# Optimization experiments

Hardware: AMD Instinct MI355X
Metric: run time of the kernel (lower is better)

The kernel has to match this reference:

```python
import jax, jax.numpy as jnp
import numpy as np

DIM = 256
HEADS = 4
HEAD_DIM = DIM // HEADS
MLP_HIDDEN = DIM * 3
B, N = 8, 4096
EPS = 1e-5


def setup_inputs() -> dict:
    key = jax.random.key(0)
    ks = jax.random.split(key, 8)
    s = 0.02
    return {
        "x": jax.random.normal(ks[0], (B, N, DIM), dtype=jnp.float32),
        "w_qkv": jax.random.normal(ks[1], (DIM, 3 * DIM), dtype=jnp.float32) * s,
        "b_qkv": jnp.zeros((3 * DIM,), dtype=jnp.float32),
        "norm_g": jnp.ones((DIM,), dtype=jnp.float32),
        "norm_b": jnp.zeros((DIM,), dtype=jnp.float32),
        "w_fc1": jax.random.normal(ks[2], (DIM, MLP_HIDDEN), dtype=jnp.float32) * s,
        "b_fc1": jnp.zeros((MLP_HIDDEN,), dtype=jnp.float32),
        "w_fc2": jax.random.normal(ks[3], (MLP_HIDDEN, DIM), dtype=jnp.float32) * s,
        "b_fc2": jnp.zeros((DIM,), dtype=jnp.float32),
    }


def _layernorm(x, g, b):
    mu = jnp.mean(x, axis=-1, keepdims=True)
    var = jnp.mean(jnp.square(x - mu), axis=-1, keepdims=True)
    return (x - mu) * jax.lax.rsqrt(var + EPS) * g + b


def reference(x, w_qkv, b_qkv, norm_g, norm_b, w_fc1, b_fc1, w_fc2, b_fc2):
    Bx, Nx, C = x.shape
    scale = HEAD_DIM ** -0.5
    qkv = (x @ w_qkv + b_qkv).reshape(Bx, Nx, 3, HEADS, HEAD_DIM)
    qkv = jnp.transpose(qkv, (2, 0, 3, 1, 4))  # [3, B, H, N, hd]
    q, k, v = qkv[0], qkv[1], qkv[2]
    k = k * scale
    # channel attention: [B,H,hd,hd]
    attn = jnp.einsum('bhnd,bhne->bhde', k, v)
    attn = jax.nn.softmax(attn, axis=-1)
    # x_feature[b,h,n,d] = sum_e attn[b,h,d,e] * q[b,h,n,e]
    xf = jnp.einsum('bhde,bhne->bhnd', attn, q)
    xf = jnp.transpose(xf, (0, 2, 1, 3)).reshape(Bx, Nx, C)
    x = x + xf
    # FFN with residual (exact GELU as torch nn.GELU default)
    h = _layernorm(x, norm_g, norm_b)
    h = jax.nn.gelu(h @ w_fc1 + b_fc1, approximate=False) @ w_fc2 + b_fc2
    return x + h
```

## Files before the change

kernel.cpp:

```cpp
#include <hip/hip_runtime.h>
#include <math.h>

typedef __bf16 bf16_t;
typedef __bf16 bf16x4 __attribute__((ext_vector_type(4)));
typedef __bf16 bf16x8 __attribute__((ext_vector_type(8)));
typedef float f32x4 __attribute__((ext_vector_type(4)));

#define DIMC 256
#define HID 768
#define NB 8
#define NN 4096
#define ROWS (NB*NN)
#define NCHUNK 16

#define AS1 __attribute__((address_space(1)))
#define AS3 __attribute__((address_space(3)))

__device__ __forceinline__ void gll16(const bf16_t* src, void* lds) {
  __builtin_amdgcn_global_load_lds((const AS1 void*)src, (AS3 void*)lds, 16, 0, 0);
}

__global__ __launch_bounds__(256) void prep_x_kernel(const float* __restrict__ x,
                                                     bf16_t* __restrict__ xb) {
  int i = (blockIdx.x * 256 + threadIdx.x) * 8;
  f32x4 a = *(const f32x4*)(x + i);
  f32x4 b = *(const f32x4*)(x + i + 4);
  bf16x8 o;
  o[0] = (bf16_t)a[0]; o[1] = (bf16_t)a[1]; o[2] = (bf16_t)a[2]; o[3] = (bf16_t)a[3];
  o[4] = (bf16_t)b[0]; o[5] = (bf16_t)b[1]; o[6] = (bf16_t)b[2]; o[7] = (bf16_t)b[3];
  *(bf16x8*)(xb + i) = o;
}

__global__ __launch_bounds__(256)
void pack_w_kernel(const float* __restrict__ w, bf16_t* __restrict__ out,
                   int K, int Nw) {
  int idx = blockIdx.x * 256 + threadIdx.x;
  int lane = idx & 63;
  int kq = (idx >> 6) % (K >> 5);
  int nt = idx / ((K >> 5) << 6);
  int n = nt * 16 + (lane & 15);
  int k0 = kq * 32 + (lane >> 4) * 8;
  bf16x8 o;
#pragma unroll
  for (int j = 0; j < 8; ++j) o[j] = (bf16_t)w[(size_t)(k0 + j) * Nw + n];
  *(bf16x8*)(out + (size_t)idx * 8) = o;
}

__device__ __forceinline__ float gelu_exact(float v) {
  return 0.5f * v * (1.0f + erff(v * 0.70710678118654752f));
}

template <int EPI>
__global__ __launch_bounds__(256, 2)
void gemm_packed_kernel(const bf16_t* __restrict__ A, const bf16_t* __restrict__ Bp,
                        const float* __restrict__ bias, bf16_t* __restrict__ outp) {
  __shared__ __align__(16) unsigned char smem[32768];
  const int tid = threadIdx.x;
  const int d = blockIdx.x + blockIdx.y * 4;
  const int w_ = (d & 7) * 256 + (d >> 3);
  const int panel = w_ & 3, rowb = w_ >> 2;
  const int m0 = rowb * 64;
  const int n0 = panel * 192;
  const int lane = tid & 63, w = tid >> 6;
  const int lr = lane & 15, lk = lane >> 4;

#pragma unroll
  for (int i = 0; i < 8; ++i) {
    int idx = i * 256 + tid;
    int row = idx >> 5, pk = idx & 31;
    gll16(A + (size_t)(m0 + row) * 256 + ((pk ^ (row & 7)) * 8), smem + idx * 16);
  }
  asm volatile("s_waitcnt vmcnt(0)" ::: "memory");
  __builtin_amdgcn_s_barrier();

  f32x4 acc[4][3] = {};
  const bf16_t* bb = Bp + (size_t)((panel * 12 + w * 3) * 8) * 512 + lane * 8;

  bf16x8 bf_c[3], af_c[4], bf_n[3], af_n[4];
#pragma unroll
  for (int nf = 0; nf < 3; ++nf) bf_c[nf] = *(const bf16x8*)(bb + (nf * 8) * 512);
#pragma unroll
  for (int mi = 0; mi < 4; ++mi) {
    int row = mi * 16 + lr;
    af_c[mi] = *(const bf16x8*)(smem + row * 512 + ((lk ^ (row & 7)) * 16));
  }

#pragma unroll
  for (int kq = 0; kq < 8; ++kq) {
    if (kq < 7) {
#pragma unroll
      for (int nf = 0; nf < 3; ++nf)
        bf_n[nf] = *(const bf16x8*)(bb + (nf * 8 + kq + 1) * 512);
#pragma unroll
      for (int mi = 0; mi < 4; ++mi) {
        int row = mi * 16 + lr;
        af_n[mi] = *(const bf16x8*)(smem + row * 512 + ((((kq + 1) * 4 + lk) ^ (row & 7)) * 16));
      }
    }
    __builtin_amdgcn_s_setprio(1);
#pragma unroll
    for (int nf = 0; nf < 3; ++nf)
#pragma unroll
      for (int mi = 0; mi < 4; ++mi)
        acc[mi][nf] = __builtin_amdgcn_mfma_f32_16x16x32_bf16(bf_c[nf], af_c[mi],
                                                              acc[mi][nf], 0, 0, 0);
    __builtin_amdgcn_s_setprio(0);
#pragma unroll
    for (int nf = 0; nf < 3; ++nf) bf_c[nf] = bf_n[nf];
#pragma unroll
    for (int mi = 0; mi < 4; ++mi) af_c[mi] = af_n[mi];
  }

  f32x4 bs[3];
#pragma unroll
  for (int nf = 0; nf < 3; ++nf)
    bs[nf] = *(const f32x4*)(bias + n0 + w * 48 + nf * 16 + lk * 4);

  __syncthreads();
#pragma unroll
  for (int mi = 0; mi < 4; ++mi) {
    int row_l = mi * 16 + lr;
#pragma unroll
    for (int nf = 0; nf < 3; ++nf) {
      int col = w * 48 + nf * 16 + lk * 4;
      f32x4 v = acc[mi][nf] + bs[nf];
      bf16x4 o;
#pragma unroll
      for (int r = 0; r < 4; ++r) {
        float val = v[r];
        if (EPI == 1) val = gelu_exact(val);
        o[r] = (bf16_t)val;
      }
      int chunk = col >> 3;
      int half = (col >> 2) & 1;
      *(bf16x4*)(smem + row_l * 384 + ((chunk ^ (row_l & 7)) << 4) + (half << 3)) = o;
    }
  }
  __syncthreads();
#pragma unroll
  for (int i = 0; i < 6; ++i) {
    int id = i * 256 + tid;
    int row_l = id / 24, c = id % 24;
    bf16x8 v = *(const bf16x8*)(smem + row_l * 384 + ((c ^ (row_l & 7)) << 4));
    *(bf16x8*)(outp + (size_t)(m0 + row_l) * 768 + n0 + c * 8) = v;
  }
}

__global__ __launch_bounds__(256, 2)
void fc2_packed_kernel(const bf16_t* __restrict__ mid, const bf16_t* __restrict__ Bp,
                       const float* __restrict__ bias, const bf16_t* __restrict__ resid,
                       float* __restrict__ outp) {
  __shared__ __align__(16) unsigned char smem[2 * 16384 + 32768];
  unsigned char* epi = smem + 32768;
  const int tid = threadIdx.x;
  const int m0 = blockIdx.x * 64;
  const int lane = tid & 63, w = tid >> 6;
  const int lr = lane & 15, lk = lane >> 4;

  auto stageA = [&](int c, int buf) {
#pragma unroll
    for (int i = 0; i < 4; ++i) {
      int idx = i * 256 + tid;
      int row = idx >> 4, pk = idx & 15;
      gll16(mid + (size_t)(m0 + row) * 768 + c * 128 + ((pk ^ (row & 7)) * 8),
            smem + buf * 16384 + idx * 16);
    }
  };

  stageA(0, 0);
  stageA(1, 1);
  asm volatile("s_waitcnt vmcnt(4)" ::: "memory");
  __builtin_amdgcn_s_barrier();

  f32x4 acc[4][4] = {};
#pragma unroll
  for (int c = 0; c < 6; ++c) {
    bf16x8 bf[4][4];
#pragma unroll
    for (int nf = 0; nf < 4; ++nf)
#pragma unroll
      for (int kql = 0; kql < 4; ++kql)
        bf[nf][kql] = *(const bf16x8*)(Bp + (size_t)((w * 4 + nf) * 24 + c * 4 + kql) * 512 + lane * 8);
    asm volatile("s_waitcnt vmcnt(0)" ::: "memory");
    __builtin_amdgcn_s_barrier();
#pragma unroll
    for (int kql = 0; kql < 4; ++kql) {
#pragma unroll
      for (int mi = 0; mi < 4; ++mi) {
        int row = mi * 16 + lr;
        bf16x8 a8 = *(const bf16x8*)(smem + (c & 1) * 16384 + row * 256 +
                                     (((kql * 4 + lk) ^ (row & 7)) * 16));
#pragma unroll
        for (int nf = 0; nf < 4; ++nf)
          acc[mi][nf] = __builtin_amdgcn_mfma_f32_16x16x32_bf16(bf[nf][kql], a8, acc[mi][nf], 0, 0, 0);
      }
    }
    __builtin_amdgcn_s_barrier();
    if (c + 2 < 6) stageA(c + 2, c & 1);
  }

  f32x4 bs[4];
#pragma unroll
  for (int nf = 0; nf < 4; ++nf)
    bs[nf] = *(const f32x4*)(bias + w * 64 + nf * 16 + lk * 4);

#pragma unroll
  for (int ph = 0; ph < 2; ++ph) {
    if (ph == 1) __syncthreads();
#pragma unroll
    for (int mj = 0; mj < 2; ++mj) {
      int mi = ph * 2 + mj;
      int row_l = mj * 16 + lr;
#pragma unroll
      for (int nf = 0; nf < 4; ++nf) {
        int cc = w * 64 + nf * 16 + lk * 4;
        f32x4 v = acc[mi][nf] + bs[nf];
        int chunk = cc >> 2;
        *(f32x4*)(epi + row_l * 1024 + ((chunk ^ (row_l & 7)) << 4)) = v;
      }
    }
    __syncthreads();
#pragma unroll
    for (int i = 0; i < 8; ++i) {
      int id = i * 256 + tid;
      int rl = id >> 6, c = id & 63;
      f32x4 v = *(const f32x4*)(epi + rl * 1024 + ((c ^ (rl & 7)) << 4));
      int grow = m0 + ph * 32 + rl;
      bf16x4 rz = *(const bf16x4*)(resid + (size_t)grow * 256 + c * 4);
#pragma unroll
      for (int r = 0; r < 4; ++r) v[r] += (float)rz[r];
      *(f32x4*)(outp + (size_t)grow * 256 + c * 4) = v;
    }
  }
}

__global__ __launch_bounds__(256)
void attn_kv_kernel(const bf16_t* __restrict__ qkv, float* __restrict__ part) {
  const int bh = blockIdx.x, chunk = blockIdx.y;
  const int b = bh >> 2, h = bh & 3;
  __shared__ __align__(16) float kl[32][68];
  __shared__ __align__(16) float vl[32][68];
  const int tid = threadIdx.x;
  const int dg = tid >> 4, eg = tid & 15;
  f32x4 acc[4] = {};
  const int n00 = chunk * (NN / NCHUNK);
  const int srow = tid >> 3, spk = tid & 7;
  for (int t = 0; t < (NN / NCHUNK) / 32; ++t) {
    int n0 = n00 + t * 32;
    {
      const bf16x8 k8 = *(const bf16x8*)(qkv + (size_t)(b * NN + n0 + srow) * HID + 256 + h * 64 + spk * 8);
      const bf16x8 v8 = *(const bf16x8*)(qkv + (size_t)(b * NN + n0 + srow) * HID + 512 + h * 64 + spk * 8);
#pragma unroll
      for (int j = 0; j < 8; ++j) kl[srow][spk * 8 + j] = (float)k8[j];
#pragma unroll
      for (int j = 0; j < 8; ++j) vl[srow][spk * 8 + j] = (float)v8[j];
    }
    __syncthreads();
#pragma unroll 8
    for (int n = 0; n < 32; ++n) {
      f32x4 k4 = *(const f32x4*)&kl[n][dg * 4];
      f32x4 v4 = *(const f32x4*)&vl[n][eg * 4];
#pragma unroll
      for (int i = 0; i < 4; ++i) acc[i] += k4[i] * v4;
    }
    __syncthreads();
  }
  float* dst = part + (size_t)(chunk * 32 + bh) * 4096;
#pragma unroll
  for (int i = 0; i < 4; ++i)
    *(f32x4*)&dst[(dg * 4 + i) * 64 + eg * 4] = acc[i];
}

__global__ __launch_bounds__(256)
void attn_softmax_kernel(const float* __restrict__ part, bf16_t* __restrict__ attnb) {
  const int bh = blockIdx.x;
  const int tid = threadIdx.x;
  const int dg = tid >> 4, eg = tid & 15;
  f32x4 s[4] = {};
  for (int c = 0; c < NCHUNK; ++c) {
    const float* src = part + (size_t)(c * 32 + bh) * 4096;
#pragma unroll
    for (int i = 0; i < 4; ++i) s[i] += *(const f32x4*)&src[(dg * 4 + i) * 64 + eg * 4];
  }
  bf16_t* dst = attnb + (size_t)bh * 4096;
#pragma unroll
  for (int i = 0; i < 4; ++i) {
    f32x4 l = s[i] * 0.125f;
    float m = fmaxf(fmaxf(l[0], l[1]), fmaxf(l[2], l[3]));
#pragma unroll
    for (int msk = 1; msk < 16; msk <<= 1) m = fmaxf(m, __shfl_xor(m, msk));
    f32x4 p;
    float sum = 0.f;
#pragma unroll
    for (int j = 0; j < 4; ++j) { p[j] = expf(l[j] - m); sum += p[j]; }
#pragma unroll
    for (int msk = 1; msk < 16; msk <<= 1) sum += __shfl_xor(sum, msk);
    float inv = 1.0f / sum;
    bf16x4 o;
#pragma unroll
    for (int j = 0; j < 4; ++j) o[j] = (bf16_t)(p[j] * inv);
    *(bf16x4*)&dst[(dg * 4 + i) * 64 + eg * 4] = o;
  }
}

__global__ __launch_bounds__(256, 2)
void xf_ln_mfma_kernel(const bf16_t* __restrict__ qkv, const bf16_t* __restrict__ attnb,
                       const bf16_t* __restrict__ xb, bf16_t* __restrict__ x2b,
                       bf16_t* __restrict__ hln, const float* __restrict__ gamma,
                       const float* __restrict__ beta) {
  __shared__ __align__(16) unsigned char qs[32768];
  __shared__ float red[4][4][16][2];
  const int tid = threadIdx.x;
  const int row0 = blockIdx.x * 64;
  const int b = row0 >> 12;
  const int lane = tid & 63, h = tid >> 6;
  const int lr = lane & 15, lk = lane >> 4;

#pragma unroll
  for (int i = 0; i < 8; ++i) {
    int idx = i * 256 + tid;
    int row = idx >> 5, pk = idx & 31;
    gll16(qkv + (size_t)(row0 + row) * HID + ((pk ^ (row & 7)) * 8), qs + idx * 16);
  }
  asm volatile("s_waitcnt vmcnt(0)" ::: "memory");
  __builtin_amdgcn_s_barrier();

  bf16x8 af[4][2];
#pragma unroll
  for (int mi = 0; mi < 4; ++mi)
#pragma unroll
    for (int kk = 0; kk < 2; ++kk) {
      int row = mi * 16 + lr;
      int pk = h * 8 + kk * 4 + lk;
      af[mi][kk] = *(const bf16x8*)(qs + row * 512 + ((pk ^ (row & 7)) * 16));
    }
  bf16x8 bfr[4][2];
#pragma unroll
  for (int nf = 0; nf < 4; ++nf)
#pragma unroll
    for (int kk = 0; kk < 2; ++kk)
      bfr[nf][kk] = *(const bf16x8*)(attnb + (size_t)(b * 4 + h) * 4096 +
                                     (nf * 16 + lr) * 64 + kk * 32 + lk * 8);
  f32x4 acc[4][4] = {};
#pragma unroll
  for (int kk = 0; kk < 2; ++kk)
#pragma unroll
    for (int mi = 0; mi < 4; ++mi)
#pragma unroll
      for (int nf = 0; nf < 4; ++nf)
        acc[mi][nf] = __builtin_amdgcn_mfma_f32_16x16x32_bf16(bfr[nf][kk], af[mi][kk], acc[mi][nf], 0, 0, 0);

  float ps[4], pq[4];
#pragma unroll
  for (int mi = 0; mi < 4; ++mi) {
    ps[mi] = 0.f; pq[mi] = 0.f;
    int row = row0 + mi * 16 + lr;
#pragma unroll
    for (int nf = 0; nf < 4; ++nf) {
      int col = h * 64 + nf * 16 + lk * 4;
      size_t off = (size_t)row * DIMC + col;
      bf16x4 xv = *(const bf16x4*)(xb + off);
      f32x4 x2;
#pragma unroll
      for (int r = 0; r < 4; ++r) {
        x2[r] = acc[mi][nf][r] + (float)xv[r];
        ps[mi] += x2[r]; pq[mi] += x2[r] * x2[r];
      }
      acc[mi][nf] = x2;
      bf16x4 o;
#pragma unroll
      for (int r = 0; r < 4; ++r) o[r] = (bf16_t)x2[r];
      *(bf16x4*)(x2b + off) = o;
    }
#pragma unroll
    for (int m = 16; m < 64; m <<= 1) {
      ps[mi] += __shfl_xor(ps[mi], m);
      pq[mi] += __shfl_xor(pq[mi], m);
    }
  }
  if (lk == 0) {
#pragma unroll
    for (int mi = 0; mi < 4; ++mi) { red[h][mi][lr][0] = ps[mi]; red[h][mi][lr][1] = pq[mi]; }
  }
  __builtin_amdgcn_s_barrier();
#pragma unroll
  for (int mi = 0; mi < 4; ++mi) {
    float t1 = red[0][mi][lr][0] + red[1][mi][lr][0] + red[2][mi][lr][0] + red[3][mi][lr][0];
    float t2 = red[0][mi][lr][1] + red[1][mi][lr][1] + red[2][mi][lr][1] + red[3][mi][lr][1];
    float mu = t1 * (1.0f / 256.0f);
    float var = t2 * (1.0f / 256.0f) - mu * mu;
    float rs = rsqrtf(var + 1e-5f);
    int row = row0 + mi * 16 + lr;
#pragma unroll
    for (int nf = 0; nf < 4; ++nf) {
      int col = h * 64 + nf * 16 + lk * 4;
      f32x4 g4 = *(const f32x4*)(gamma + col);
      f32x4 b4 = *(const f32x4*)(beta + col);
      bf16x4 o;
#pragma unroll
      for (int r = 0; r < 4; ++r)
        o[r] = (bf16_t)((acc[mi][nf][r] - mu) * rs * g4[r] + b4[r]);
      *(bf16x4*)(hln + (size_t)row * DIMC + col) = o;
    }
  }
}

extern "C" void kernel_launch(void* const* d_in, const int* in_sizes, int n_in,
                              void* d_out, int out_size, void* d_ws, size_t ws_size,
                              hipStream_t stream) {
  const float* x      = (const float*)d_in[0];
  const float* w_qkv  = (const float*)d_in[1];
  const float* b_qkv  = (const float*)d_in[2];
  const float* norm_g = (const float*)d_in[3];
  const float* norm_b = (const float*)d_in[4];
  const float* w_fc1  = (const float*)d_in[5];
  const float* b_fc1  = (const float*)d_in[6];
  const float* w_fc2  = (const float*)d_in[7];
  const float* b_fc2  = (const float*)d_in[8];

  char* ws = (char*)d_ws;
  size_t off = 0;
  bf16_t* qkv   = (bf16_t*)(ws + off); off += (size_t)ROWS * HID * 2;
  bf16_t* mid   = qkv;
  bf16_t* xb    = (bf16_t*)(ws + off); off += (size_t)ROWS * DIMC * 2;
  bf16_t* hln   = (bf16_t*)(ws + off); off += (size_t)ROWS * DIMC * 2;
  bf16_t* x2b   = (bf16_t*)(ws + off); off += (size_t)ROWS * DIMC * 2;
  float*  part  = (float*)(ws + off);  off += (size_t)NCHUNK * 32 * 4096 * 4;
  bf16_t* attnb = (bf16_t*)(ws + off); off += (size_t)32 * 4096 * 2;
  bf16_t* Bq    = (bf16_t*)(ws + off); off += (size_t)768 * 256 * 2;
  bf16_t* B1    = (bf16_t*)(ws + off); off += (size_t)768 * 256 * 2;
  bf16_t* B2    = (bf16_t*)(ws + off); off += (size_t)256 * 768 * 2;

  prep_x_kernel<<<(ROWS * DIMC) / (256 * 8), 256, 0, stream>>>(x, xb);
  pack_w_kernel<<<96, 256, 0, stream>>>(w_qkv, Bq, 256, 768);
  pack_w_kernel<<<96, 256, 0, stream>>>(w_fc1, B1, 256, 768);
  pack_w_kernel<<<96, 256, 0, stream>>>(w_fc2, B2, 768, 256);

  gemm_packed_kernel<0><<<dim3(4, ROWS / 64), 256, 0, stream>>>(xb, Bq, b_qkv, qkv);
  attn_kv_kernel<<<dim3(32, NCHUNK), 256, 0, stream>>>(qkv, part);
  attn_softmax_kernel<<<32, 256, 0, stream>>>(part, attnb);
  xf_ln_mfma_kernel<<<ROWS / 64, 256, 0, stream>>>(qkv, attnb, xb, x2b, hln, norm_g, norm_b);
  gemm_packed_kernel<1><<<dim3(4, ROWS / 64), 256, 0, stream>>>(hln, B1, b_fc1, mid);
  fc2_packed_kernel<<<ROWS / 64, 256, 0, stream>>>(mid, B2, b_fc2, x2b, (float*)d_out);
}
```

Measured before the change: 130.4 us.

## Fuse prep kernels, deepen B-fragment prefetch in GEMM, double attention chunks

Merges the x-to-bf16 conversion and the three weight-packing kernels into a single launch, removing three kernel launches and their gaps. The packed GEMM now prefetches B fragments two k-steps ahead using a triple-buffered register array instead of copying next-to-current each step, which is meant to hide global-load latency. NCHUNK is raised from 16 to 32, doubling the parallelism of the KV-reduction kernel but also the size of the partial buffer the softmax kernel has to reduce. Register pressure in the GEMM rises, which could hurt occupancy at the two-blocks-per-SIMD launch bound.

```diff
diff --git a/kernel.cpp b/kernel.cpp
--- a/kernel.cpp
+++ b/kernel.cpp
@@ -11,7 +11,7 @@
 #define NB 8
 #define NN 4096
 #define ROWS (NB*NN)
-#define NCHUNK 16
+#define NCHUNK 32
 
 #define AS1 __attribute__((address_space(1)))
 #define AS3 __attribute__((address_space(3)))
@@ -20,21 +20,12 @@
   __builtin_amdgcn_global_load_lds((const AS1 void*)src, (AS3 void*)lds, 16, 0, 0);
 }
 
-__global__ __launch_bounds__(256) void prep_x_kernel(const float* __restrict__ x,
-                                                     bf16_t* __restrict__ xb) {
-  int i = (blockIdx.x * 256 + threadIdx.x) * 8;
-  f32x4 a = *(const f32x4*)(x + i);
-  f32x4 b = *(const f32x4*)(x + i + 4);
-  bf16x8 o;
-  o[0] = (bf16_t)a[0]; o[1] = (bf16_t)a[1]; o[2] = (bf16_t)a[2]; o[3] = (bf16_t)a[3];
-  o[4] = (bf16_t)b[0]; o[5] = (bf16_t)b[1]; o[6] = (bf16_t)b[2]; o[7] = (bf16_t)b[3];
-  *(bf16x8*)(xb + i) = o;
-}
-
-__global__ __launch_bounds__(256)
-void pack_w_kernel(const float* __restrict__ w, bf16_t* __restrict__ out,
-                   int K, int Nw) {
-  int idx = blockIdx.x * 256 + threadIdx.x;
+__device__ __forceinline__ float gelu_exact(float v) {
+  return 0.5f * v * (1.0f + erff(v * 0.70710678118654752f));
+}
+
+__device__ __forceinline__ void pack_w_body(int idx, const float* __restrict__ w,
+                                            bf16_t* __restrict__ out, int K, int Nw) {
   int lane = idx & 63;
   int kq = (idx >> 6) % (K >> 5);
   int nt = idx / ((K >> 5) << 6);
@@ -46,8 +37,27 @@
   *(bf16x8*)(out + (size_t)idx * 8) = o;
 }
 
-__device__ __forceinline__ float gelu_exact(float v) {
-  return 0.5f * v * (1.0f + erff(v * 0.70710678118654752f));
+__global__ __launch_bounds__(256)
+void prep_all_kernel(const float* __restrict__ x, bf16_t* __restrict__ xb,
+                     const float* __restrict__ w_qkv, bf16_t* __restrict__ Bq,
+                     const float* __restrict__ w_fc1, bf16_t* __restrict__ B1,
+                     const float* __restrict__ w_fc2, bf16_t* __restrict__ B2) {
+  const int bid = blockIdx.x, tid = threadIdx.x;
+  if (bid < 4096) {
+    int i = (bid * 256 + tid) * 8;
+    f32x4 a = *(const f32x4*)(x + i);
+    f32x4 b = *(const f32x4*)(x + i + 4);
+    bf16x8 o;
+    o[0] = (bf16_t)a[0]; o[1] = (bf16_t)a[1]; o[2] = (bf16_t)a[2]; o[3] = (bf16_t)a[3];
+    o[4] = (bf16_t)b[0]; o[5] = (bf16_t)b[1]; o[6] = (bf16_t)b[2]; o[7] = (bf16_t)b[3];
+    *(bf16x8*)(xb + i) = o;
+  } else if (bid < 4192) {
+    pack_w_body((bid - 4096) * 256 + tid, w_qkv, Bq, 256, 768);
+  } else if (bid < 4288) {
+    pack_w_body((bid - 4192) * 256 + tid, w_fc1, B1, 256, 768);
+  } else {
+    pack_w_body((bid - 4288) * 256 + tid, w_fc2, B2, 768, 256);
+  }
 }
 
 template <int EPI>
@@ -76,25 +86,32 @@
   f32x4 acc[4][3] = {};
   const bf16_t* bb = Bp + (size_t)((panel * 12 + w * 3) * 8) * 512 + lane * 8;
 
-  bf16x8 bf_c[3], af_c[4], bf_n[3], af_n[4];
-#pragma unroll
-  for (int nf = 0; nf < 3; ++nf) bf_c[nf] = *(const bf16x8*)(bb + (nf * 8) * 512);
+  bf16x8 bf[3][3];
+  bf16x8 af[2][4];
+#pragma unroll
+  for (int nf = 0; nf < 3; ++nf) {
+    bf[0][nf] = *(const bf16x8*)(bb + (nf * 8 + 0) * 512);
+    bf[1][nf] = *(const bf16x8*)(bb + (nf * 8 + 1) * 512);
+  }
 #pragma unroll
   for (int mi = 0; mi < 4; ++mi) {
     int row = mi * 16 + lr;
-    af_c[mi] = *(const bf16x8*)(smem + row * 512 + ((lk ^ (row & 7)) * 16));
+    af[0][mi] = *(const bf16x8*)(smem + row * 512 + ((lk ^ (row & 7)) * 16));
   }
 
 #pragma unroll
   for (int kq = 0; kq < 8; ++kq) {
+    if (kq < 6) {
+#pragma unroll
+      for (int nf = 0; nf < 3; ++nf)
+        bf[(kq + 2) % 3][nf] = *(const bf16x8*)(bb + (nf * 8 + kq + 2) * 512);
+    }
     if (kq < 7) {
-#pragma unroll
-      for (int nf = 0; nf < 3; ++nf)
-        bf_n[nf] = *(const bf16x8*)(bb + (nf * 8 + kq + 1) * 512);
 #pragma unroll
       for (int mi = 0; mi < 4; ++mi) {
         int row = mi * 16 + lr;
-        af_n[mi] = *(const bf16x8*)(smem + row * 512 + ((((kq + 1) * 4 + lk) ^ (row & 7)) * 16));
+        af[(kq + 1) & 1][mi] =
+            *(const bf16x8*)(smem + row * 512 + ((((kq + 1) * 4 + lk) ^ (row & 7)) * 16));
       }
     }
     __builtin_amdgcn_s_setprio(1);
@@ -102,13 +119,9 @@
     for (int nf = 0; nf < 3; ++nf)
 #pragma unroll
       for (int mi = 0; mi < 4; ++mi)
-        acc[mi][nf] = __builtin_amdgcn_mfma_f32_16x16x32_bf16(bf_c[nf], af_c[mi],
+        acc[mi][nf] = __builtin_amdgcn_mfma_f32_16x16x32_bf16(bf[kq % 3][nf], af[kq & 1][mi],
                                                               acc[mi][nf], 0, 0, 0);
     __builtin_amdgcn_s_setprio(0);
-#pragma unroll
-    for (int nf = 0; nf < 3; ++nf) bf_c[nf] = bf_n[nf];
-#pragma unroll
-    for (int mi = 0; mi < 4; ++mi) af_c[mi] = af_n[mi];
   }
 
   f32x4 bs[3];
@@ -431,10 +444,7 @@
   bf16_t* B1    = (bf16_t*)(ws + off); off += (size_t)768 * 256 * 2;
   bf16_t* B2    = (bf16_t*)(ws + off); off += (size_t)256 * 768 * 2;
 
-  prep_x_kernel<<<(ROWS * DIMC) / (256 * 8), 256, 0, stream>>>(x, xb);
-  pack_w_kernel<<<96, 256, 0, stream>>>(w_qkv, Bq, 256, 768);
-  pack_w_kernel<<<96, 256, 0, stream>>>(w_fc1, B1, 256, 768);
-  pack_w_kernel<<<96, 256, 0, stream>>>(w_fc2, B2, 768, 256);
+  prep_all_kernel<<<4384, 256, 0, stream>>>(x, xb, w_qkv, Bq, w_fc1, B1, w_fc2, B2);
 
   gemm_packed_kernel<0><<<dim3(4, ROWS / 64), 256, 0, stream>>>(xb, Bq, b_qkv, qkv);
   attn_kv_kernel<<<dim3(32, NCHUNK), 256, 0, stream>>>(qkv, part);
```

Result: faster. 125.3 us (-3.9%).
